# Performance work log

Measured on AMD Instinct MI355X. Metric: run time of the kernel, lower is better.

Reference implementation:

```python
import jax, jax.numpy as jnp
import numpy as np

N = 10           # node count hardcoded in original module
FEAT_IN = 3      # position(2) + orientation(1)
FEAT_OUT = 16    # 'simple' mode
FEAT_CC = 2 * FEAT_OUT
B = 16384
NEG_SLOPE = 0.2


def _pair_index():
    # Faithful pair ordering: for node i, row 0 is the self-pair (i,i),
    # rows 1..N-1 are j != i in ascending order.
    idx = np.empty((N, N), dtype=np.int32)
    for i in range(N):
        idx[i, 0] = i
        idx[i, 1:] = [j for j in range(N) if j != i]
    return jnp.asarray(idx)


def setup_inputs() -> dict:
    key = jax.random.key(0)
    ks = jax.random.split(key, 12)
    s = 0.1
    return {
        "position": jax.random.normal(ks[0], (B, N, 2), dtype=jnp.float32),
        "orientation": jax.random.normal(ks[1], (B, N, 1), dtype=jnp.float32),
        # preliminary_transform: Linear(3 -> 16)
        "Wp": jax.random.normal(ks[2], (FEAT_IN, FEAT_OUT), dtype=jnp.float32) * s,
        "bp": jax.random.normal(ks[3], (FEAT_OUT,), dtype=jnp.float32) * s,
        # connectivity_net: Linear(32->32), LReLU, Linear(32->8), LReLU, Linear(8->2)
        "W1": jax.random.normal(ks[4], (FEAT_CC, 32), dtype=jnp.float32) * s,
        "b1": jax.random.normal(ks[5], (32,), dtype=jnp.float32) * s,
        "W2": jax.random.normal(ks[6], (32, 8), dtype=jnp.float32) * s,
        "b2": jax.random.normal(ks[7], (8,), dtype=jnp.float32) * s,
        "W3": jax.random.normal(ks[8], (8, 2), dtype=jnp.float32) * s,
        "b3": jax.random.normal(ks[9], (2,), dtype=jnp.float32) * s,
    }


def reference(position, orientation, Wp, bp, W1, b1, W2, b2, W3, b3):
    lrelu = lambda x: jnp.where(x >= 0, x, NEG_SLOPE * x)
    # [B, N, 3] -> [B, N, 16]
    feat = jnp.concatenate([position, orientation], axis=2) @ Wp + bp
    idx = _pair_index()                                   # [N, N]
    vj = feat[:, idx]                                     # [B, N, N, 16] gathered partners
    vi = jnp.broadcast_to(feat[:, :, None, :], vj.shape)  # [B, N, N, 16] source node
    pair = jnp.concatenate([vi, vj], axis=-1)             # [B, N, N, 32]
    h = lrelu(pair @ W1 + b1)
    h = lrelu(h @ W2 + b2)
    big_edge = h @ W3 + b3                                # [B, N, N, 2]
    adjacency = jnp.argmax(big_edge, axis=3)              # [B, N, N]
    return big_edge, adjacency
```

## Files before the change

kernel.cpp:

```cpp
#include <hip/hip_runtime.h>


typedef float v2f __attribute__((ext_vector_type(2)));
typedef float v4f __attribute__((ext_vector_type(4)));

constexpr int G = 12;
constexpr int GB_STRIDE = 36;
constexpr float NEG = 0.2f;

__global__ __launch_bounds__(256, 1) void fuse_kernel(
    const float* __restrict__ Wp, const float* __restrict__ bp,
    const float* __restrict__ W1, const float* __restrict__ b1,
    float* __restrict__ ws)
{
    const int t = threadIdx.x;
    if (t < 192) {
        const int d = t >> 6, k = t & 63;
        const int kk = k & 31;
        const int fo = (k < 32) ? 0 : 16;
        float acc = 0.f;
#pragma unroll
        for (int f = 0; f < 16; ++f)
            acc = fmaf(Wp[d * 16 + f], W1[(fo + f) * 32 + kk], acc);
        ws[d * 64 + k] = acc;
    } else {
        const int k = t - 192;
        const int kk = k & 31;
        const int fo = (k < 32) ? 0 : 16;
        float acc = 0.f;
#pragma unroll
        for (int f = 0; f < 16; ++f)
            acc = fmaf(bp[f], W1[(fo + f) * 32 + kk], acc);
        if (k < 32) acc += b1[k];
        ws[192 + k] = acc;
    }
}

__global__ __launch_bounds__(128, 3) void gpn_kernel(
    const float* __restrict__ pos,
    const float* __restrict__ ori,
    const float* __restrict__ ws,
    const float* __restrict__ W2,
    const float* __restrict__ b2,
    const float* __restrict__ W3,
    const float* __restrict__ b3,
    float* __restrict__ out,
    int B)
{
    __shared__ float sgb[G * 10 * GB_STRIDE];

    const int t = threadIdx.x;
    const int bBase = blockIdx.x * G;
    const int remG = B - bBase;
    const int nRows = ((remG < G) ? remG : G) * 10;

    const v4f* m4 = (const v4f*)ws;
    const v4f* c4 = (const v4f*)(ws + 192);

    v4f ga[8];
    const int r = t;
    const int g = r / 10;
    const int i = r - g * 10;
    if (r < nRows) {
        const int node = bBase * 10 + r;
        const v2f p = ((const v2f*)pos)[node];
        const float o = ori[node];
        v4f* dst = (v4f*)&sgb[r * GB_STRIDE];
#pragma unroll
        for (int q = 0; q < 8; ++q) {
            v4f gg = c4[q];
            gg += p.x * m4[q];
            gg += p.y * m4[16 + q];
            gg += o   * m4[32 + q];
            ga[q] = gg;
        }
#pragma unroll
        for (int q = 8; q < 16; ++q) {
            v4f gg = c4[q];
            gg += p.x * m4[q];
            gg += p.y * m4[16 + q];
            gg += o   * m4[32 + q];
            dst[q - 8] = gg;
        }
    }
    __syncthreads();

    if (r < nRows) {
        const v2f* w2p = (const v2f*)W2;
        const v2f* w3p = (const v2f*)W3;
        const v2f bb2_0 = ((const v2f*)b2)[0];
        const v2f bb2_1 = ((const v2f*)b2)[1];
        const v2f bb2_2 = ((const v2f*)b2)[2];
        const v2f bb2_3 = ((const v2f*)b2)[3];
        const v2f bb3   = ((const v2f*)b3)[0];

        const float* gbase = &sgb[(g * 10) * GB_STRIDE];

        v2f A[10][4];
#pragma unroll
        for (int j = 0; j < 10; ++j) {
            A[j][0] = bb2_0; A[j][1] = bb2_1; A[j][2] = bb2_2; A[j][3] = bb2_3;
        }

#pragma unroll
        for (int q = 0; q < 8; ++q) {
            const v4f gaq = ga[q];
            const int k0 = 4 * q;
            const v2f w00 = w2p[4 * (k0 + 0) + 0], w01 = w2p[4 * (k0 + 0) + 1],
                      w02 = w2p[4 * (k0 + 0) + 2], w03 = w2p[4 * (k0 + 0) + 3];
            const v2f w10 = w2p[4 * (k0 + 1) + 0], w11 = w2p[4 * (k0 + 1) + 1],
                      w12 = w2p[4 * (k0 + 1) + 2], w13 = w2p[4 * (k0 + 1) + 3];
            const v2f w20 = w2p[4 * (k0 + 2) + 0], w21 = w2p[4 * (k0 + 2) + 1],
                      w22 = w2p[4 * (k0 + 2) + 2], w23 = w2p[4 * (k0 + 2) + 3];
            const v2f w30 = w2p[4 * (k0 + 3) + 0], w31 = w2p[4 * (k0 + 3) + 1],
                      w32 = w2p[4 * (k0 + 3) + 2], w33 = w2p[4 * (k0 + 3) + 3];
#pragma unroll
            for (int j = 0; j < 10; ++j) {
                const v4f gb = *(const v4f*)(gbase + j * GB_STRIDE + 4 * q);
                const v4f s = gaq + gb;
                const v4f h = __builtin_elementwise_max(s, s * NEG);
                A[j][0] += h.x * w00; A[j][1] += h.x * w01;
                A[j][2] += h.x * w02; A[j][3] += h.x * w03;
                A[j][0] += h.y * w10; A[j][1] += h.y * w11;
                A[j][2] += h.y * w12; A[j][3] += h.y * w13;
                A[j][0] += h.z * w20; A[j][1] += h.z * w21;
                A[j][2] += h.z * w22; A[j][3] += h.z * w23;
                A[j][0] += h.w * w30; A[j][1] += h.w * w31;
                A[j][2] += h.w * w32; A[j][3] += h.w * w33;
            }
        }

        const int eRow = (bBase + g) * 100 + i * 10;
        const size_t adjOff = (size_t)B * 200;
#pragma unroll
        for (int j = 0; j < 10; ++j) {
            const v2f h20 = __builtin_elementwise_max(A[j][0], A[j][0] * NEG);
            const v2f h21 = __builtin_elementwise_max(A[j][1], A[j][1] * NEG);
            const v2f h22 = __builtin_elementwise_max(A[j][2], A[j][2] * NEG);
            const v2f h23 = __builtin_elementwise_max(A[j][3], A[j][3] * NEG);

            v2f ev = bb3;
            ev += h20.x * w3p[0];
            ev += h20.y * w3p[1];
            ev += h21.x * w3p[2];
            ev += h21.y * w3p[3];
            ev += h22.x * w3p[4];
            ev += h22.y * w3p[5];
            ev += h23.x * w3p[6];
            ev += h23.y * w3p[7];

            const int c = (j == i) ? 0 : ((j < i) ? (j + 1) : j);
            const int E = eRow + c;
            ((v2f*)out)[E] = ev;
            out[adjOff + E] = (ev.y > ev.x) ? 1.0f : 0.0f;
        }
    }
}

extern "C" void kernel_launch(void* const* d_in, const int* in_sizes, int n_in,
                              void* d_out, int out_size, void* d_ws, size_t ws_size,
                              hipStream_t stream) {
    const float* pos = (const float*)d_in[0];
    const float* ori = (const float*)d_in[1];
    const float* Wp  = (const float*)d_in[2];
    const float* bp  = (const float*)d_in[3];
    const float* W1  = (const float*)d_in[4];
    const float* b1  = (const float*)d_in[5];
    const float* W2  = (const float*)d_in[6];
    const float* b2  = (const float*)d_in[7];
    const float* W3  = (const float*)d_in[8];
    const float* b3  = (const float*)d_in[9];
    float* out = (float*)d_out;
    float* ws  = (float*)d_ws;

    const int B = in_sizes[0] / 20;
    const int nBlocks = (B + G - 1) / G;

    fuse_kernel<<<1, 256, 0, stream>>>(Wp, bp, W1, b1, ws);
    gpn_kernel<<<nBlocks, 128, 0, stream>>>(pos, ori, ws, W2, b2, W3, b3, out, B);
}
```

Baseline: 98.53 us.

## Stage outputs in LDS and write coalesced nontemporal vector stores

Each block now handles 24 batch items with 256 threads instead of 12 with 128. Edge and adjacency results go into reused shared memory first, and the block then writes them with contiguous float4 nontemporal stores. This replaces the scattered per-thread 8-byte and 4-byte global writes. In exchange it adds two extra barriers and the LDS round trip, and occupancy may change because launch bounds move to 256 threads and 2 blocks.

Measured after the change: 94.95 us. -3.6%, faster.

```diff
diff --git a/kernel.cpp b/kernel.cpp
--- a/kernel.cpp
+++ b/kernel.cpp
@@ -4,9 +4,13 @@
 typedef float v2f __attribute__((ext_vector_type(2)));
 typedef float v4f __attribute__((ext_vector_type(4)));
 
-constexpr int G = 12;
+constexpr int G = 24;
 constexpr int GB_STRIDE = 36;
 constexpr float NEG = 0.2f;
+
+constexpr int SGB_FLOATS = G * 10 * GB_STRIDE;
+constexpr int RES_E_FLOATS = G * 200;
+constexpr int RES_A_FLOATS = G * 100;
 
 __global__ __launch_bounds__(256, 1) void fuse_kernel(
     const float* __restrict__ Wp, const float* __restrict__ bp,
@@ -36,7 +40,7 @@
     }
 }
 
-__global__ __launch_bounds__(128, 3) void gpn_kernel(
+__global__ __launch_bounds__(256, 2) void gpn_kernel(
     const float* __restrict__ pos,
     const float* __restrict__ ori,
     const float* __restrict__ ws,
@@ -47,12 +51,13 @@
     float* __restrict__ out,
     int B)
 {
-    __shared__ float sgb[G * 10 * GB_STRIDE];
+    __shared__ float sL[SGB_FLOATS];
 
     const int t = threadIdx.x;
     const int bBase = blockIdx.x * G;
-    const int remG = B - bBase;
-    const int nRows = ((remG < G) ? remG : G) * 10;
+    const int remG0 = B - bBase;
+    const int remG = (remG0 < G) ? remG0 : G;
+    const int nRows = remG * 10;
 
     const v4f* m4 = (const v4f*)ws;
     const v4f* c4 = (const v4f*)(ws + 192);
@@ -65,7 +70,7 @@
         const int node = bBase * 10 + r;
         const v2f p = ((const v2f*)pos)[node];
         const float o = ori[node];
-        v4f* dst = (v4f*)&sgb[r * GB_STRIDE];
+        v4f* dst = (v4f*)&sL[r * GB_STRIDE];
 #pragma unroll
         for (int q = 0; q < 8; ++q) {
             v4f gg = c4[q];
@@ -85,18 +90,16 @@
     }
     __syncthreads();
 
+    v2f A[10][4];
     if (r < nRows) {
         const v2f* w2p = (const v2f*)W2;
-        const v2f* w3p = (const v2f*)W3;
         const v2f bb2_0 = ((const v2f*)b2)[0];
         const v2f bb2_1 = ((const v2f*)b2)[1];
         const v2f bb2_2 = ((const v2f*)b2)[2];
         const v2f bb2_3 = ((const v2f*)b2)[3];
-        const v2f bb3   = ((const v2f*)b3)[0];
-
-        const float* gbase = &sgb[(g * 10) * GB_STRIDE];
-
-        v2f A[10][4];
+
+        const float* gbase = &sL[(g * 10) * GB_STRIDE];
+
 #pragma unroll
         for (int j = 0; j < 10; ++j) {
             A[j][0] = bb2_0; A[j][1] = bb2_1; A[j][2] = bb2_2; A[j][3] = bb2_3;
@@ -129,9 +132,14 @@
                 A[j][2] += h.w * w32; A[j][3] += h.w * w33;
             }
         }
-
-        const int eRow = (bBase + g) * 100 + i * 10;
-        const size_t adjOff = (size_t)B * 200;
+    }
+    __syncthreads();
+
+    float* res_e = sL;
+    float* res_a = sL + RES_E_FLOATS;
+    if (r < nRows) {
+        const v2f* w3p = (const v2f*)W3;
+        const v2f bb3 = ((const v2f*)b3)[0];
 #pragma unroll
         for (int j = 0; j < 10; ++j) {
             const v2f h20 = __builtin_elementwise_max(A[j][0], A[j][0] * NEG);
@@ -150,10 +158,25 @@
             ev += h23.y * w3p[7];
 
             const int c = (j == i) ? 0 : ((j < i) ? (j + 1) : j);
-            const int E = eRow + c;
-            ((v2f*)out)[E] = ev;
-            out[adjOff + E] = (ev.y > ev.x) ? 1.0f : 0.0f;
-        }
+            const int eIdx = r * 10 + c;
+            *(v2f*)&res_e[eIdx * 2] = ev;
+            res_a[eIdx] = (ev.y > ev.x) ? 1.0f : 0.0f;
+        }
+    }
+    __syncthreads();
+
+    {
+        const int nV4e = remG * 50;
+        const v4f* se = (const v4f*)res_e;
+        v4f* oe = (v4f*)(out + (size_t)bBase * 200);
+        for (int idx = t; idx < nV4e; idx += 256)
+            __builtin_nontemporal_store(se[idx], &oe[idx]);
+
+        const int nV4a = remG * 25;
+        const v4f* sa = (const v4f*)res_a;
+        v4f* oa = (v4f*)(out + (size_t)B * 200 + (size_t)bBase * 100);
+        for (int idx = t; idx < nV4a; idx += 256)
+            __builtin_nontemporal_store(sa[idx], &oa[idx]);
     }
 }
 
@@ -177,5 +200,5 @@
     const int nBlocks = (B + G - 1) / G;
 
     fuse_kernel<<<1, 256, 0, stream>>>(Wp, bp, W1, b1, ws);
-    gpn_kernel<<<nBlocks, 128, 0, stream>>>(pos, ori, ws, W2, b2, W3, b3, out, B);
+    gpn_kernel<<<nBlocks, 256, 0, stream>>>(pos, ori, ws, W2, b2, W3, b3, out, B);
 }
```

## Map one thread per edge and drop shared-memory node precompute

Applied to the files above, without the earlier changes.

Replaces the per-node thread design, where each thread looped over ten partners using shared-memory projected features, with one thread per edge. Each thread recomputes the first-layer pre-activation directly from both nodes' raw inputs via split fused weight matrices. Outputs are written contiguously with nontemporal stores. This targets the uncoalesced strided writes and the low thread count of the old layout, at the cost of recomputing node projections about ten times per node and more global loads of position and orientation.

New measurement: 96.28 us. -2.3%, faster.

```diff
diff --git a/kernel.cpp b/kernel.cpp
--- a/kernel.cpp
+++ b/kernel.cpp
@@ -4,8 +4,6 @@
 typedef float v2f __attribute__((ext_vector_type(2)));
 typedef float v4f __attribute__((ext_vector_type(4)));
 
-constexpr int G = 12;
-constexpr int GB_STRIDE = 36;
 constexpr float NEG = 0.2f;
 
 __global__ __launch_bounds__(256, 1) void fuse_kernel(
@@ -14,29 +12,32 @@
     float* __restrict__ ws)
 {
     const int t = threadIdx.x;
-    if (t < 192) {
-        const int d = t >> 6, k = t & 63;
-        const int kk = k & 31;
-        const int fo = (k < 32) ? 0 : 16;
+    if (t < 96) {
+        const int d = t >> 5, k = t & 31;
         float acc = 0.f;
 #pragma unroll
         for (int f = 0; f < 16; ++f)
-            acc = fmaf(Wp[d * 16 + f], W1[(fo + f) * 32 + kk], acc);
-        ws[d * 64 + k] = acc;
-    } else {
-        const int k = t - 192;
-        const int kk = k & 31;
-        const int fo = (k < 32) ? 0 : 16;
+            acc = fmaf(Wp[d * 16 + f], W1[f * 32 + k], acc);
+        ws[d * 32 + k] = acc;
+    } else if (t < 192) {
+        const int u = t - 96;
+        const int d = u >> 5, k = u & 31;
         float acc = 0.f;
 #pragma unroll
         for (int f = 0; f < 16; ++f)
-            acc = fmaf(bp[f], W1[(fo + f) * 32 + kk], acc);
-        if (k < 32) acc += b1[k];
+            acc = fmaf(Wp[d * 16 + f], W1[(16 + f) * 32 + k], acc);
+        ws[96 + d * 32 + k] = acc;
+    } else if (t < 224) {
+        const int k = t - 192;
+        float acc = b1[k];
+#pragma unroll
+        for (int f = 0; f < 16; ++f)
+            acc = fmaf(bp[f], W1[f * 32 + k] + W1[(16 + f) * 32 + k], acc);
         ws[192 + k] = acc;
     }
 }
 
-__global__ __launch_bounds__(128, 3) void gpn_kernel(
+__global__ __launch_bounds__(256, 5) void gpn_kernel(
     const float* __restrict__ pos,
     const float* __restrict__ ori,
     const float* __restrict__ ws,
@@ -47,114 +48,84 @@
     float* __restrict__ out,
     int B)
 {
-    __shared__ float sgb[G * 10 * GB_STRIDE];
+    const int e = blockIdx.x * 256 + threadIdx.x;
+    if (e >= B * 100) return;
 
-    const int t = threadIdx.x;
-    const int bBase = blockIdx.x * G;
-    const int remG = B - bBase;
-    const int nRows = ((remG < G) ? remG : G) * 10;
+    const unsigned ue = (unsigned)e;
+    const unsigned b  = ue / 100u;
+    const unsigned rem = ue - b * 100u;
+    const unsigned i  = rem / 10u;
+    const unsigned c  = rem - i * 10u;
+    const unsigned j  = (c == 0u) ? i : (((c - 1u) < i) ? (c - 1u) : c);
 
-    const v4f* m4 = (const v4f*)ws;
-    const v4f* c4 = (const v4f*)(ws + 192);
+    const v2f pi = ((const v2f*)pos)[b * 10u + i];
+    const v2f pj = ((const v2f*)pos)[b * 10u + j];
+    const float oi = ori[b * 10u + i];
+    const float oj = ori[b * 10u + j];
 
-    v4f ga[8];
-    const int r = t;
-    const int g = r / 10;
-    const int i = r - g * 10;
-    if (r < nRows) {
-        const int node = bBase * 10 + r;
-        const v2f p = ((const v2f*)pos)[node];
-        const float o = ori[node];
-        v4f* dst = (v4f*)&sgb[r * GB_STRIDE];
+    const v4f* Ma = (const v4f*)ws;
+    const v4f* Mb = (const v4f*)(ws + 96);
+    const v4f* cc = (const v4f*)(ws + 192);
+
+    v4f h[8];
 #pragma unroll
-        for (int q = 0; q < 8; ++q) {
-            v4f gg = c4[q];
-            gg += p.x * m4[q];
-            gg += p.y * m4[16 + q];
-            gg += o   * m4[32 + q];
-            ga[q] = gg;
-        }
+    for (int q = 0; q < 8; ++q) {
+        v4f s = cc[q];
+        s += pi.x * Ma[q];
+        s += pi.y * Ma[8 + q];
+        s += oi   * Ma[16 + q];
+        s += pj.x * Mb[q];
+        s += pj.y * Mb[8 + q];
+        s += oj   * Mb[16 + q];
+        h[q] = __builtin_elementwise_max(s, s * NEG);
+    }
+
+    const v2f* w2p = (const v2f*)W2;
+    v2f a0 = ((const v2f*)b2)[0];
+    v2f a1 = ((const v2f*)b2)[1];
+    v2f a2 = ((const v2f*)b2)[2];
+    v2f a3 = ((const v2f*)b2)[3];
 #pragma unroll
-        for (int q = 8; q < 16; ++q) {
-            v4f gg = c4[q];
-            gg += p.x * m4[q];
-            gg += p.y * m4[16 + q];
-            gg += o   * m4[32 + q];
-            dst[q - 8] = gg;
-        }
+    for (int q = 0; q < 8; ++q) {
+        const v4f hh = h[q];
+        const int k0 = 4 * q;
+        a0 += hh.x * w2p[4 * (k0 + 0) + 0];
+        a1 += hh.x * w2p[4 * (k0 + 0) + 1];
+        a2 += hh.x * w2p[4 * (k0 + 0) + 2];
+        a3 += hh.x * w2p[4 * (k0 + 0) + 3];
+        a0 += hh.y * w2p[4 * (k0 + 1) + 0];
+        a1 += hh.y * w2p[4 * (k0 + 1) + 1];
+        a2 += hh.y * w2p[4 * (k0 + 1) + 2];
+        a3 += hh.y * w2p[4 * (k0 + 1) + 3];
+        a0 += hh.z * w2p[4 * (k0 + 2) + 0];
+        a1 += hh.z * w2p[4 * (k0 + 2) + 1];
+        a2 += hh.z * w2p[4 * (k0 + 2) + 2];
+        a3 += hh.z * w2p[4 * (k0 + 2) + 3];
+        a0 += hh.w * w2p[4 * (k0 + 3) + 0];
+        a1 += hh.w * w2p[4 * (k0 + 3) + 1];
+        a2 += hh.w * w2p[4 * (k0 + 3) + 2];
+        a3 += hh.w * w2p[4 * (k0 + 3) + 3];
     }
-    __syncthreads();
 
-    if (r < nRows) {
-        const v2f* w2p = (const v2f*)W2;
-        const v2f* w3p = (const v2f*)W3;
-        const v2f bb2_0 = ((const v2f*)b2)[0];
-        const v2f bb2_1 = ((const v2f*)b2)[1];
-        const v2f bb2_2 = ((const v2f*)b2)[2];
-        const v2f bb2_3 = ((const v2f*)b2)[3];
-        const v2f bb3   = ((const v2f*)b3)[0];
+    const v2f* w3p = (const v2f*)W3;
+    const v2f h20 = __builtin_elementwise_max(a0, a0 * NEG);
+    const v2f h21 = __builtin_elementwise_max(a1, a1 * NEG);
+    const v2f h22 = __builtin_elementwise_max(a2, a2 * NEG);
+    const v2f h23 = __builtin_elementwise_max(a3, a3 * NEG);
 
-        const float* gbase = &sgb[(g * 10) * GB_STRIDE];
+    v2f ev = ((const v2f*)b3)[0];
+    ev += h20.x * w3p[0];
+    ev += h20.y * w3p[1];
+    ev += h21.x * w3p[2];
+    ev += h21.y * w3p[3];
+    ev += h22.x * w3p[4];
+    ev += h22.y * w3p[5];
+    ev += h23.x * w3p[6];
+    ev += h23.y * w3p[7];
 
-        v2f A[10][4];
-#pragma unroll
-        for (int j = 0; j < 10; ++j) {
-            A[j][0] = bb2_0; A[j][1] = bb2_1; A[j][2] = bb2_2; A[j][3] = bb2_3;
-        }
-
-#pragma unroll
-        for (int q = 0; q < 8; ++q) {
-            const v4f gaq = ga[q];
-            const int k0 = 4 * q;
-            const v2f w00 = w2p[4 * (k0 + 0) + 0], w01 = w2p[4 * (k0 + 0) + 1],
-                      w02 = w2p[4 * (k0 + 0) + 2], w03 = w2p[4 * (k0 + 0) + 3];
-            const v2f w10 = w2p[4 * (k0 + 1) + 0], w11 = w2p[4 * (k0 + 1) + 1],
-                      w12 = w2p[4 * (k0 + 1) + 2], w13 = w2p[4 * (k0 + 1) + 3];
-            const v2f w20 = w2p[4 * (k0 + 2) + 0], w21 = w2p[4 * (k0 + 2) + 1],
-                      w22 = w2p[4 * (k0 + 2) + 2], w23 = w2p[4 * (k0 + 2) + 3];
-            const v2f w30 = w2p[4 * (k0 + 3) + 0], w31 = w2p[4 * (k0 + 3) + 1],
-                      w32 = w2p[4 * (k0 + 3) + 2], w33 = w2p[4 * (k0 + 3) + 3];
-#pragma unroll
-            for (int j = 0; j < 10; ++j) {
-                const v4f gb = *(const v4f*)(gbase + j * GB_STRIDE + 4 * q);
-                const v4f s = gaq + gb;
-                const v4f h = __builtin_elementwise_max(s, s * NEG);
-                A[j][0] += h.x * w00; A[j][1] += h.x * w01;
-                A[j][2] += h.x * w02; A[j][3] += h.x * w03;
-                A[j][0] += h.y * w10; A[j][1] += h.y * w11;
-                A[j][2] += h.y * w12; A[j][3] += h.y * w13;
-                A[j][0] += h.z * w20; A[j][1] += h.z * w21;
-                A[j][2] += h.z * w22; A[j][3] += h.z * w23;
-                A[j][0] += h.w * w30; A[j][1] += h.w * w31;
-                A[j][2] += h.w * w32; A[j][3] += h.w * w33;
-            }
-        }
-
-        const int eRow = (bBase + g) * 100 + i * 10;
-        const size_t adjOff = (size_t)B * 200;
-#pragma unroll
-        for (int j = 0; j < 10; ++j) {
-            const v2f h20 = __builtin_elementwise_max(A[j][0], A[j][0] * NEG);
-            const v2f h21 = __builtin_elementwise_max(A[j][1], A[j][1] * NEG);
-            const v2f h22 = __builtin_elementwise_max(A[j][2], A[j][2] * NEG);
-            const v2f h23 = __builtin_elementwise_max(A[j][3], A[j][3] * NEG);
-
-            v2f ev = bb3;
-            ev += h20.x * w3p[0];
-            ev += h20.y * w3p[1];
-            ev += h21.x * w3p[2];
-            ev += h21.y * w3p[3];
-            ev += h22.x * w3p[4];
-            ev += h22.y * w3p[5];
-            ev += h23.x * w3p[6];
-            ev += h23.y * w3p[7];
-
-            const int c = (j == i) ? 0 : ((j < i) ? (j + 1) : j);
-            const int E = eRow + c;
-            ((v2f*)out)[E] = ev;
-            out[adjOff + E] = (ev.y > ev.x) ? 1.0f : 0.0f;
-        }
-    }
+    __builtin_nontemporal_store(ev, &((v2f*)out)[e]);
+    const float av = (ev.y > ev.x) ? 1.0f : 0.0f;
+    __builtin_nontemporal_store(av, &out[(size_t)B * 200 + e]);
 }
 
 extern "C" void kernel_launch(void* const* d_in, const int* in_sizes, int n_in,
@@ -174,8 +145,9 @@
     float* ws  = (float*)d_ws;
 
     const int B = in_sizes[0] / 20;
-    const int nBlocks = (B + G - 1) / G;
+    const int nEdges = B * 100;
+    const int nBlocks = (nEdges + 255) / 256;
 
     fuse_kernel<<<1, 256, 0, stream>>>(Wp, bp, W1, b1, ws);
-    gpn_kernel<<<nBlocks, 128, 0, stream>>>(pos, ori, ws, W2, b2, W3, b3, out, B);
+    gpn_kernel<<<nBlocks, 256, 0, stream>>>(pos, ori, ws, W2, b2, W3, b3, out, B);
 }
```
